# Kernel optimization log

Hardware: AMD Instinct MI355X
Metric: run time of the kernel (lower is better)

Reference implementation:

```python
import jax, jax.numpy as jnp
import numpy as np

INPUT_DIM = 2048
NUM_EXPERTS = 64
TOP_K = 8
BATCH = 16384


def setup_inputs() -> dict:
    key = jax.random.key(0)
    k_x, k_n, k_wg, k_bg, k_wn = jax.random.split(key, 5)
    x = jax.random.normal(k_x, (BATCH, INPUT_DIM), dtype=jnp.float32)
    noise = jax.random.normal(k_n, (BATCH, NUM_EXPERTS), dtype=jnp.float32)
    Wg = jax.random.normal(k_wg, (NUM_EXPERTS, INPUT_DIM), dtype=jnp.float32) * 0.02
    bg = jax.random.normal(k_bg, (NUM_EXPERTS,), dtype=jnp.float32) * 0.02
    Wn = jax.random.normal(k_wn, (NUM_EXPERTS, INPUT_DIM), dtype=jnp.float32) * 0.02
    return {"x": x, "noise": noise, "Wg": Wg, "bg": bg, "Wn": Wn}


def reference(x, noise, Wg, bg, Wn):
    # logits: (B, E)
    logits = jnp.einsum("bd,ed->be", x, Wg) + bg
    noise_stddev = jax.nn.softplus(jnp.einsum("bd,ed->be", x, Wn))
    noisy_logits = logits + noise * noise_stddev

    top_k_values, top_k_indices = jax.lax.top_k(noisy_logits, TOP_K)  # (B, K)
    top_k_weights = jax.nn.softmax(top_k_values, axis=-1)

    # aux losses
    dispatch = jnp.argmax(noisy_logits, axis=-1)            # (B,)
    f = jax.nn.one_hot(dispatch, NUM_EXPERTS, dtype=logits.dtype).mean(axis=0)  # (E,)
    p = jax.nn.softmax(logits, axis=-1).mean(axis=0)        # (E,)
    load_balance_loss = NUM_EXPERTS * jnp.sum(f * p)
    z_loss = jnp.mean(jax.nn.logsumexp(logits, axis=-1) ** 2)

    return top_k_weights, top_k_indices, load_balance_loss, z_loss
```

## Files before the change

kernel.cpp:

```cpp
#include <hip/hip_runtime.h>
#include <math.h>

#define IDIM 2048
#define NE   64
#define TOPK 8
#define NB   16384
#define BM   32
#define BK   64
#define NCH  (IDIM / BK)
#define KH   1024
#define NCHH 16
#define TAU  2.5e-4f

#define WS_CNT 129
#define WS_LIST 130
#define WSPLIT_BYTE 66560
#define WSPLIT_REQ  (WSPLIT_BYTE + NCH * 32768)
#define PART0_BYTE  (WSPLIT_BYTE + NCH * 32768)
#define PART1_BYTE  (PART0_BYTE + (size_t)NB * 128 * 4)
#define SPLIT_REQ   (PART1_BYTE + (size_t)NB * 128 * 4)

typedef __attribute__((ext_vector_type(8))) short bf16x8_t;
typedef __attribute__((ext_vector_type(4))) float f32x4_t;

__device__ __forceinline__ float softplusf(float v) {
    return (v > 0.f) ? (v + log1pf(expf(-v))) : log1pf(expf(v));
}
__device__ __forceinline__ double softplus_d(double v) {
    return (v > 0.0) ? (v + log1p(exp(-v))) : log1p(exp(v));
}

__device__ __forceinline__ short f2bf(float f) {
    unsigned u = __float_as_uint(f);
    unsigned r = (u + 0x7FFFu + ((u >> 16) & 1u)) >> 16;
    return (short)r;
}
__device__ __forceinline__ float bf2f(short s) {
    return __uint_as_float(((unsigned)(unsigned short)s) << 16);
}

__global__ void init_ws_kernel(float* ws) {
    int t = threadIdx.x;
    if (t < WS_LIST) ws[t] = 0.0f;
}

__device__ __forceinline__ void split8(const float4 v0, const float4 v1,
                                       bf16x8_t& H, bf16x8_t& L) {
    float fv[8] = {v0.x, v0.y, v0.z, v0.w, v1.x, v1.y, v1.z, v1.w};
    #pragma unroll
    for (int q = 0; q < 8; ++q) {
        short hb = f2bf(fv[q]);
        short lb = f2bf(fv[q] - bf2f(hb));
        H[q] = hb; L[q] = lb;
    }
}

__device__ __forceinline__ void cvt_slot(const float4 v0, const float4 v1,
                                         char* hiP, char* loP, int off) {
    bf16x8_t H, L;
    split8(v0, v1, H, L);
    *(bf16x8_t*)(hiP + off) = H;
    *(bf16x8_t*)(loP + off) = L;
}

__global__ __launch_bounds__(256) void prep_kernel(
    const float* __restrict__ Wg, const float* __restrict__ Wn,
    char* __restrict__ wsW, float* __restrict__ ws)
{
    if (blockIdx.x == 128) {
        if (threadIdx.x < WS_LIST) ws[threadIdx.x] = 0.0f;
        return;
    }
    int g = blockIdx.x * 256 + threadIdx.x;
    int t = g >> 10, i = g & 1023;
    int row = i >> 3, wslot = i & 7;
    int kslot = wslot ^ (row & 7);
    const float* src = (row < 64 ? Wg + (size_t)row * IDIM
                                 : Wn + (size_t)(row - 64) * IDIM) + t * BK + kslot * 8;
    float4 v0 = *(const float4*)src;
    float4 v1 = *(const float4*)(src + 4);
    bf16x8_t H, L;
    split8(v0, v1, H, L);
    char* dst = wsW + (size_t)t * 32768;
    *(bf16x8_t*)(dst + i * 16)         = H;
    *(bf16x8_t*)(dst + 16384 + i * 16) = L;
}

__global__ __launch_bounds__(512, 4) void gemm_half_kernel(
    const float* __restrict__ x, const char* __restrict__ wsW,
    float* __restrict__ part0, float* __restrict__ part1)
{
    __shared__ char smem[40960] __attribute__((aligned(16)));
    char* AH = smem;
    char* AL = smem + 4096;
    char* BH = smem + 8192;
    char* BL = smem + 24576;

    const int u   = threadIdx.x;
    const int w   = u >> 6;
    const int l   = u & 63;
    const int lr  = l & 15;
    const int lg4 = l >> 4;
    const int s7  = lr & 7;
    const int half = blockIdx.x & 1;
    const int row0 = (blockIdx.x >> 1) * BM;
    float* pb = half ? part1 : part0;

    const int ar  = (u >> 3) & 31;
    const int ac  = u & 7;
    const int aoff = ar * 128 + (((ac ^ (ar & 7)) & 7) << 4);
    const float* pa = x + (size_t)(row0 + ar) * IDIM + half * KH + ac * 8;

    f32x4_t acc[2];
    #pragma unroll
    for (int mt = 0; mt < 2; ++mt) {
        f32x4_t z = {0.f, 0.f, 0.f, 0.f};
        acc[mt] = z;
    }

    float4 ra0, ra1;
    int4 w0, w1, w2, w3;

#define HLOADT(tt) { const int k0 = (tt) * BK;                                  \
    if (u < 256) { ra0 = *(const float4*)(pa + k0);                             \
                   ra1 = *(const float4*)(pa + k0 + 4); }                       \
    const char* s_ = wsW + (size_t)(half * NCHH + (tt)) * 32768 + u * 16;       \
    w0 = *(const int4*)(s_);          w1 = *(const int4*)(s_ + 8192);           \
    w2 = *(const int4*)(s_ + 16384);  w3 = *(const int4*)(s_ + 24576); }

    HLOADT(0);

    for (int t = 0; t < NCHH; ++t) {
        __syncthreads();
        if (u < 256) cvt_slot(ra0, ra1, AH, AL, aoff);
        *(int4*)(BH + u * 16)        = w0;
        *(int4*)(BH + 8192 + u * 16) = w1;
        *(int4*)(BL + u * 16)        = w2;
        *(int4*)(BL + 8192 + u * 16) = w3;
        if (t + 1 < NCHH) HLOADT(t + 1);
        __syncthreads();

        #pragma unroll
        for (int ks = 0; ks < 2; ++ks) {
            const int so = (((ks * 4 + lg4) ^ s7) << 4);
            bf16x8_t ah[2], al_[2], bh, bl;
            #pragma unroll
            for (int mt = 0; mt < 2; ++mt) {
                const int o = (mt * 16 + lr) * 128 + so;
                ah[mt]  = *(const bf16x8_t*)(AH + o);
                al_[mt] = *(const bf16x8_t*)(AL + o);
            }
            {
                const int o = (w * 16 + lr) * 128 + so;
                bh = *(const bf16x8_t*)(BH + o);
                bl = *(const bf16x8_t*)(BL + o);
            }
            #pragma unroll
            for (int mt = 0; mt < 2; ++mt) {
                acc[mt] = __builtin_amdgcn_mfma_f32_16x16x32_bf16(ah[mt],  bh, acc[mt], 0, 0, 0);
                acc[mt] = __builtin_amdgcn_mfma_f32_16x16x32_bf16(ah[mt],  bl, acc[mt], 0, 0, 0);
                acc[mt] = __builtin_amdgcn_mfma_f32_16x16x32_bf16(al_[mt], bh, acc[mt], 0, 0, 0);
            }
        }
    }

    #pragma unroll
    for (int mt = 0; mt < 2; ++mt)
        #pragma unroll
        for (int r = 0; r < 4; ++r)
            pb[(size_t)(row0 + mt * 16 + lg4 * 4 + r) * 128 + (w * 16 + lr)] = acc[mt][r];
}

__global__ __launch_bounds__(512) void gating_kernel(
    const float* __restrict__ part0, const float* __restrict__ part1,
    const float* __restrict__ noise, const float* __restrict__ bg,
    float* __restrict__ out_w, float* __restrict__ out_i,
    float* __restrict__ ws, int listCap)
{
    __shared__ float sP[NE];
    __shared__ float sF[NE];
    __shared__ float sZ[1];
    const int u = threadIdx.x;
    const int w = u >> 6, l = u & 63;
    const int row0 = blockIdx.x * 32;

    if (u < NE) { sP[u] = 0.f; sF[u] = 0.f; }
    if (u == 0) sZ[0] = 0.f;
    __syncthreads();

    float pacc = 0.f, zacc = 0.f;
    #pragma unroll 1
    for (int rr = 0; rr < 4; ++rr) {
        const int grow = row0 + w * 4 + rr;
        float lg   = part0[(size_t)grow * 128 + l] + part1[(size_t)grow * 128 + l] + bg[l];
        float npre = part0[(size_t)grow * 128 + 64 + l] + part1[(size_t)grow * 128 + 64 + l];
        float vcur = fmaf(noise[(size_t)grow * NE + l], softplusf(npre), lg);

        float tkv[9]; int tki[9];
        #pragma unroll
        for (int k = 0; k < 9; ++k) {
            float mv = vcur; int mi = l;
            #pragma unroll
            for (int o = 32; o > 0; o >>= 1) {
                float ov = __shfl_xor(mv, o);
                int   oi = __shfl_xor(mi, o);
                if (ov > mv || (ov == mv && oi < mi)) { mv = ov; mi = oi; }
            }
            tkv[k] = mv; tki[k] = mi;
            if (l == mi) vcur = -1e30f;
        }

        float m0 = tkv[0], s = 0.f, wk[TOPK];
        #pragma unroll
        for (int k = 0; k < TOPK; ++k) { wk[k] = expf(tkv[k] - m0); s += wk[k]; }
        float inv = 1.f / s;
        float myw = 0.f; int myi = 0;
        #pragma unroll
        for (int k = 0; k < TOPK; ++k)
            if (l == k) { myw = wk[k] * inv; myi = tki[k]; }
        if (l < TOPK) {
            out_w[(size_t)grow * TOPK + l] = myw;
            out_i[(size_t)grow * TOPK + l] = (float)myi;
        }

        if (l == 0) {
            atomicAdd(&sF[tki[0]], 1.f);
            float ming = 1e30f;
            #pragma unroll
            for (int k = 0; k < 8; ++k) ming = fminf(ming, tkv[k] - tkv[k + 1]);
            if (ming < TAU) {
                int slot = atomicAdd((int*)&ws[WS_CNT], 1);
                if (slot < listCap) ((int*)ws)[WS_LIST + slot] = grow;
            }
        }

        float rm = lg;
        #pragma unroll
        for (int o = 32; o > 0; o >>= 1) rm = fmaxf(rm, __shfl_xor(rm, o));
        float pe = expf(lg - rm);
        float ssum = pe;
        #pragma unroll
        for (int o = 32; o > 0; o >>= 1) ssum += __shfl_xor(ssum, o);
        pacc += pe / ssum;
        if (l == 0) { float lse = rm + logf(ssum); zacc += lse * lse; }
    }

    atomicAdd(&sP[l], pacc);
    if (l == 0) atomicAdd(sZ, zacc);
    __syncthreads();
    if (u < NE) {
        atomicAdd(&ws[u],      sF[u]);
        atomicAdd(&ws[NE + u], sP[u]);
    }
    if (u == 0) atomicAdd(&ws[2 * NE], sZ[0]);
}

template<bool PRE>
__global__ __launch_bounds__(512, 4) void gate_main_kernel(
    const float* __restrict__ x, const float* __restrict__ noise,
    const float* __restrict__ Wg, const float* __restrict__ bg,
    const float* __restrict__ Wn, const char* __restrict__ wsW,
    float* __restrict__ out_w, float* __restrict__ out_i,
    float* __restrict__ ws, int listCap)
{
    __shared__ char smem[41488] __attribute__((aligned(16)));
    char* AH = smem;
    char* AL = smem + 4096;
    char* BH = smem + 8192;
    char* BL = smem + 24576;
    float* sP = (float*)(smem + 40960);
    float* sF = (float*)(smem + 41216);
    float* sZ = (float*)(smem + 41472);
    float* sL = (float*)smem;

    const int u   = threadIdx.x;
    const int w   = u >> 6;
    const int l   = u & 63;
    const int lr  = l & 15;
    const int lg4 = l >> 4;
    const int s7  = lr & 7;
    const int row0 = blockIdx.x * BM;

    if (u < NE) { sP[u] = 0.f; sF[u] = 0.f; }
    if (u == 0) sZ[0] = 0.f;

    const int ar  = (u >> 3) & 31;
    const int ac  = u & 7;
    const int aoff = ar * 128 + (((ac ^ (ar & 7)) & 7) << 4);
    const float* pa = x + (size_t)(row0 + ar) * IDIM + ac * 8;

    const int br  = u >> 3;
    const float* pg = Wg + (size_t)br * IDIM + ac * 8;
    const float* pn = Wn + (size_t)br * IDIM + ac * 8;
    const int woff = br * 128 + ((ac ^ (br & 7)) << 4);

    f32x4_t acc[2];
    #pragma unroll
    for (int mt = 0; mt < 2; ++mt) {
        f32x4_t z = {0.f, 0.f, 0.f, 0.f};
        acc[mt] = z;
    }

    float4 ra0, ra1;
    int4 w0, w1, w2, w3;
    float4 g0, g1, n0, n1;

#define LOADT(tt) { const int k0 = (tt) * BK;                                   \
    if (u < 256) { ra0 = *(const float4*)(pa + k0);                             \
                   ra1 = *(const float4*)(pa + k0 + 4); }                       \
    if constexpr (PRE) {                                                        \
        const char* s_ = wsW + (size_t)(tt) * 32768 + u * 16;                   \
        w0 = *(const int4*)(s_);          w1 = *(const int4*)(s_ + 8192);       \
        w2 = *(const int4*)(s_ + 16384);  w3 = *(const int4*)(s_ + 24576);      \
    } else {                                                                    \
        g0 = *(const float4*)(pg + k0);   g1 = *(const float4*)(pg + k0 + 4);   \
        n0 = *(const float4*)(pn + k0);   n1 = *(const float4*)(pn + k0 + 4);   \
    } }

    LOADT(0);

    for (int t = 0; t < NCH; ++t) {
        __syncthreads();
        if (u < 256) cvt_slot(ra0, ra1, AH, AL, aoff);
        if constexpr (PRE) {
            *(int4*)(BH + u * 16)        = w0;
            *(int4*)(BH + 8192 + u * 16) = w1;
            *(int4*)(BL + u * 16)        = w2;
            *(int4*)(BL + 8192 + u * 16) = w3;
        } else {
            cvt_slot(g0, g1, BH, BL, woff);
            cvt_slot(n0, n1, BH, BL, woff + 8192);
        }
        if (t + 1 < NCH) LOADT(t + 1);
        __syncthreads();

        #pragma unroll
        for (int ks = 0; ks < 2; ++ks) {
            const int so = (((ks * 4 + lg4) ^ s7) << 4);
            bf16x8_t ah[2], al_[2], bh, bl;
            #pragma unroll
            for (int mt = 0; mt < 2; ++mt) {
                const int o = (mt * 16 + lr) * 128 + so;
                ah[mt]  = *(const bf16x8_t*)(AH + o);
                al_[mt] = *(const bf16x8_t*)(AL + o);
            }
            {
                const int o = (w * 16 + lr) * 128 + so;
                bh = *(const bf16x8_t*)(BH + o);
                bl = *(const bf16x8_t*)(BL + o);
            }
            #pragma unroll
            for (int mt = 0; mt < 2; ++mt) {
                acc[mt] = __builtin_amdgcn_mfma_f32_16x16x32_bf16(ah[mt],  bh, acc[mt], 0, 0, 0);
                acc[mt] = __builtin_amdgcn_mfma_f32_16x16x32_bf16(ah[mt],  bl, acc[mt], 0, 0, 0);
                acc[mt] = __builtin_amdgcn_mfma_f32_16x16x32_bf16(al_[mt], bh, acc[mt], 0, 0, 0);
            }
        }
    }
    __syncthreads();

    #pragma unroll
    for (int mt = 0; mt < 2; ++mt)
        #pragma unroll
        for (int r = 0; r < 4; ++r)
            sL[(mt * 16 + lg4 * 4 + r) * 132 + (w * 16 + lr)] = acc[mt][r];
    __syncthreads();

    float pacc = 0.f, zacc = 0.f;
    #pragma unroll 1
    for (int rr = 0; rr < 4; ++rr) {
        const int r = w * 4 + rr;
        const int grow = row0 + r;
        float lg   = sL[r * 132 + l] + bg[l];
        float npre = sL[r * 132 + 64 + l];
        float vcur = fmaf(noise[(size_t)grow * NE + l], softplusf(npre), lg);

        float tkv[9]; int tki[9];
        #pragma unroll
        for (int k = 0; k < 9; ++k) {
            float mv = vcur; int mi = l;
            #pragma unroll
            for (int o = 32; o > 0; o >>= 1) {
                float ov = __shfl_xor(mv, o);
                int   oi = __shfl_xor(mi, o);
                if (ov > mv || (ov == mv && oi < mi)) { mv = ov; mi = oi; }
            }
            tkv[k] = mv; tki[k] = mi;
            if (l == mi) vcur = -1e30f;
        }

        float m0 = tkv[0], s = 0.f, wk[TOPK];
        #pragma unroll
        for (int k = 0; k < TOPK; ++k) { wk[k] = expf(tkv[k] - m0); s += wk[k]; }
        float inv = 1.f / s;
        float myw = 0.f; int myi = 0;
        #pragma unroll
        for (int k = 0; k < TOPK; ++k)
            if (l == k) { myw = wk[k] * inv; myi = tki[k]; }
        if (l < TOPK) {
            out_w[(size_t)grow * TOPK + l] = myw;
            out_i[(size_t)grow * TOPK + l] = (float)myi;
        }

        if (l == 0) {
            atomicAdd(&sF[tki[0]], 1.f);
            float ming = 1e30f;
            #pragma unroll
            for (int k = 0; k < 8; ++k) ming = fminf(ming, tkv[k] - tkv[k + 1]);
            if (ming < TAU) {
                int slot = atomicAdd((int*)&ws[WS_CNT], 1);
                if (slot < listCap) ((int*)ws)[WS_LIST + slot] = grow;
            }
        }

        float rm = lg;
        #pragma unroll
        for (int o = 32; o > 0; o >>= 1) rm = fmaxf(rm, __shfl_xor(rm, o));
        float pe = expf(lg - rm);
        float ssum = pe;
        #pragma unroll
        for (int o = 32; o > 0; o >>= 1) ssum += __shfl_xor(ssum, o);
        pacc += pe / ssum;
        if (l == 0) { float lse = rm + logf(ssum); zacc += lse * lse; }
    }

    atomicAdd(&sP[l], pacc);
    if (l == 0) atomicAdd(sZ, zacc);
    __syncthreads();
    if (u < NE) {
        atomicAdd(&ws[u],      sF[u]);
        atomicAdd(&ws[NE + u], sP[u]);
    }
    if (u == 0) atomicAdd(&ws[2 * NE], sZ[0]);
}

__global__ __launch_bounds__(512) void recheck_finalize_kernel(
    const float* __restrict__ x, const float* __restrict__ noise,
    const float* __restrict__ Wg, const float* __restrict__ bg,
    const float* __restrict__ Wn,
    float* __restrict__ out_w, float* __restrict__ out_i, float* __restrict__ out_s,
    const float* __restrict__ ws, int listCap)
{
    __shared__ double sRed[1024];
    const int t = threadIdx.x;

    if (blockIdx.x == 0 && t < 64) {
        float v = (ws[t] / (float)NB) * (ws[NE + t] / (float)NB);
        #pragma unroll
        for (int o = 32; o > 0; o >>= 1) v += __shfl_down(v, o);
        if (t == 0) {
            out_s[0] = (float)NE * v;
            out_s[1] = ws[2 * NE] / (float)NB;
        }
    }

    const int* wsi = (const int*)ws;
    int cnt = wsi[WS_CNT];
    if (cnt > listCap) cnt = listCap;
    if (cnt <= 0) return;

    const int slot = t & 127;
    const int q4   = t >> 7;
    const float* wrb = ((slot < 64) ? (Wg + (size_t)slot * IDIM)
                                    : (Wn + (size_t)(slot - 64) * IDIM)) + q4 * 512;

    const int npair = (cnt + 1) >> 1;
    for (int bi = blockIdx.x; bi < npair; bi += gridDim.x) {
        const int i1 = 2 * bi + 1;
        const int r0 = wsi[WS_LIST + 2 * bi];
        const int r1 = wsi[WS_LIST + (i1 < cnt ? i1 : cnt - 1)];
        const float* x0 = x + (size_t)r0 * IDIM + q4 * 512;
        const float* x1 = x + (size_t)r1 * IDIM + q4 * 512;

        double a0 = 0.0, a1 = 0.0;
        #pragma unroll 4
        for (int k = 0; k < 512; k += 4) {
            float4 wv  = *(const float4*)(wrb + k);
            float4 xv0 = *(const float4*)(x0 + k);
            float4 xv1 = *(const float4*)(x1 + k);
            a0 = fma((double)xv0.x, (double)wv.x, a0);
            a1 = fma((double)xv1.x, (double)wv.x, a1);
            a0 = fma((double)xv0.y, (double)wv.y, a0);
            a1 = fma((double)xv1.y, (double)wv.y, a1);
            a0 = fma((double)xv0.z, (double)wv.z, a0);
            a1 = fma((double)xv1.z, (double)wv.z, a1);
            a0 = fma((double)xv0.w, (double)wv.w, a0);
            a1 = fma((double)xv1.w, (double)wv.w, a1);
        }
        sRed[t * 2]     = a0;
        sRed[t * 2 + 1] = a1;
        __syncthreads();
        if (t < 128) {
            #pragma unroll
            for (int i = 0; i < 2; ++i)
                sRed[t * 2 + i] = sRed[t * 2 + i] + sRed[(t + 128) * 2 + i]
                                + sRed[(t + 256) * 2 + i] + sRed[(t + 384) * 2 + i];
        }
        __syncthreads();

        if (t < 64) {
            const int lane = t;
            const double bgl = (double)bg[lane];
            #pragma unroll 1
            for (int i = 0; i < 2; ++i) {
                const int row = i ? r1 : r0;
                double g = sRed[lane * 2 + i];
                double n = sRed[(64 + lane) * 2 + i];
                double lgd = g + bgl;
                double nz = (double)noise[(size_t)row * NE + lane];
                double vcur = fma(nz, softplus_d(n), lgd);

                double tkv[TOPK]; int tki[TOPK];
                #pragma unroll
                for (int k = 0; k < TOPK; ++k) {
                    double mv = vcur; int mi = lane;
                    #pragma unroll
                    for (int o = 32; o > 0; o >>= 1) {
                        double ov = __shfl_xor(mv, o);
                        int    oi = __shfl_xor(mi, o);
                        if (ov > mv || (ov == mv && oi < mi)) { mv = ov; mi = oi; }
                    }
                    tkv[k] = mv; tki[k] = mi;
                    if (lane == mi) vcur = -1e300;
                }
                double m0 = tkv[0], s = 0.0, wk[TOPK];
                #pragma unroll
                for (int k = 0; k < TOPK; ++k) { wk[k] = exp(tkv[k] - m0); s += wk[k]; }
                double inv = 1.0 / s;
                float myw = 0.f; int myi = 0;
                #pragma unroll
                for (int k = 0; k < TOPK; ++k)
                    if (lane == k) { myw = (float)(wk[k] * inv); myi = tki[k]; }
                if (lane < TOPK) {
                    out_w[(size_t)row * TOPK + lane] = myw;
                    out_i[(size_t)row * TOPK + lane] = (float)myi;
                }
            }
        }
        __syncthreads();
    }
}

extern "C" void kernel_launch(void* const* d_in, const int* in_sizes, int n_in,
                              void* d_out, int out_size, void* d_ws, size_t ws_size,
                              hipStream_t stream) {
    const float* x     = (const float*)d_in[0];
    const float* noise = (const float*)d_in[1];
    const float* Wg    = (const float*)d_in[2];
    const float* bg    = (const float*)d_in[3];
    const float* Wn    = (const float*)d_in[4];
    float* out = (float*)d_out;
    float* ws  = (float*)d_ws;
    char*  wsW = (char*)d_ws + WSPLIT_BYTE;

    long cap = (long)(ws_size / 4) - WS_LIST;
    int listCap = (int)(cap < 0 ? 0 : (cap > NB ? NB : cap));
    const bool pre   = ws_size >= (size_t)WSPLIT_REQ;
    const bool split = ws_size >= (size_t)SPLIT_REQ;

    if (split) {
        float* part0 = (float*)((char*)d_ws + PART0_BYTE);
        float* part1 = (float*)((char*)d_ws + PART1_BYTE);
        hipLaunchKernelGGL(prep_kernel, dim3(129), dim3(256), 0, stream, Wg, Wn, wsW, ws);
        hipLaunchKernelGGL(gemm_half_kernel, dim3(2 * NB / BM), dim3(512), 0, stream,
                           x, wsW, part0, part1);
        hipLaunchKernelGGL(gating_kernel, dim3(NB / 32), dim3(512), 0, stream,
                           part0, part1, noise, bg,
                           out, out + (size_t)NB * TOPK, ws, listCap);
    } else if (pre) {
        hipLaunchKernelGGL(prep_kernel, dim3(129), dim3(256), 0, stream, Wg, Wn, wsW, ws);
        hipLaunchKernelGGL(gate_main_kernel<true>, dim3(NB / BM), dim3(512), 0, stream,
                           x, noise, Wg, bg, Wn, wsW,
                           out, out + (size_t)NB * TOPK, ws, listCap);
    } else {
        hipLaunchKernelGGL(init_ws_kernel, dim3(1), dim3(256), 0, stream, ws);
        hipLaunchKernelGGL(gate_main_kernel<false>, dim3(NB / BM), dim3(512), 0, stream,
                           x, noise, Wg, bg, Wn, wsW,
                           out, out + (size_t)NB * TOPK, ws, listCap);
    }
    hipLaunchKernelGGL(recheck_finalize_kernel, dim3(1024), dim3(512), 0, stream,
                       x, noise, Wg, bg, Wn,
                       out, out + (size_t)NB * TOPK, out + 2 * (size_t)NB * TOPK,
                       ws, listCap);
}
```

Baseline: 144.8 us.

## Split GEMM reduction dimension into four parts and widen recheck blocks

The split-K GEMM now splits the 2048-wide reduction into four 512-wide slices instead of two, launching four times as many blocks per row tile, each doing half as many K chunks. The gating kernel sums four partial buffers, which doubles partial-result traffic in exchange for more parallelism. The recheck/finalize kernel moves to 1024-thread blocks, each thread covering 256 K elements, and does an 8-way shared reduction. TAU drops to 1e-4, which changes how many rows are flagged for the fp64 recheck and could shrink the recheck list.

```diff
diff --git a/kernel.cpp b/kernel.cpp
--- a/kernel.cpp
+++ b/kernel.cpp
@@ -8,17 +8,17 @@
 #define BM   32
 #define BK   64
 #define NCH  (IDIM / BK)
-#define KH   1024
-#define NCHH 16
-#define TAU  2.5e-4f
+#define NQ   4
+#define KQ   512
+#define NCHQ 8
+#define TAU  1e-4f
 
 #define WS_CNT 129
 #define WS_LIST 130
 #define WSPLIT_BYTE 66560
 #define WSPLIT_REQ  (WSPLIT_BYTE + NCH * 32768)
-#define PART0_BYTE  (WSPLIT_BYTE + NCH * 32768)
-#define PART1_BYTE  (PART0_BYTE + (size_t)NB * 128 * 4)
-#define SPLIT_REQ   (PART1_BYTE + (size_t)NB * 128 * 4)
+#define PART_BYTE   (WSPLIT_BYTE + NCH * 32768)
+#define SPLIT_REQ   (PART_BYTE + (size_t)NQ * NB * 128 * 4)
 
 typedef __attribute__((ext_vector_type(8))) short bf16x8_t;
 typedef __attribute__((ext_vector_type(4))) float f32x4_t;
@@ -86,9 +86,9 @@
     *(bf16x8_t*)(dst + 16384 + i * 16) = L;
 }
 
-__global__ __launch_bounds__(512, 4) void gemm_half_kernel(
+__global__ __launch_bounds__(512, 4) void gemm_quarter_kernel(
     const float* __restrict__ x, const char* __restrict__ wsW,
-    float* __restrict__ part0, float* __restrict__ part1)
+    float* __restrict__ part)
 {
     __shared__ char smem[40960] __attribute__((aligned(16)));
     char* AH = smem;
@@ -102,14 +102,14 @@
     const int lr  = l & 15;
     const int lg4 = l >> 4;
     const int s7  = lr & 7;
-    const int half = blockIdx.x & 1;
-    const int row0 = (blockIdx.x >> 1) * BM;
-    float* pb = half ? part1 : part0;
+    const int q   = blockIdx.x & 3;
+    const int row0 = (blockIdx.x >> 2) * BM;
+    float* pb = part + (size_t)q * NB * 128;
 
     const int ar  = (u >> 3) & 31;
     const int ac  = u & 7;
     const int aoff = ar * 128 + (((ac ^ (ar & 7)) & 7) << 4);
-    const float* pa = x + (size_t)(row0 + ar) * IDIM + half * KH + ac * 8;
+    const float* pa = x + (size_t)(row0 + ar) * IDIM + q * KQ + ac * 8;
 
     f32x4_t acc[2];
     #pragma unroll
@@ -121,23 +121,23 @@
     float4 ra0, ra1;
     int4 w0, w1, w2, w3;
 
-#define HLOADT(tt) { const int k0 = (tt) * BK;                                  \
+#define QLOADT(tt) { const int k0 = (tt) * BK;                                  \
     if (u < 256) { ra0 = *(const float4*)(pa + k0);                             \
                    ra1 = *(const float4*)(pa + k0 + 4); }                       \
-    const char* s_ = wsW + (size_t)(half * NCHH + (tt)) * 32768 + u * 16;       \
+    const char* s_ = wsW + (size_t)(q * NCHQ + (tt)) * 32768 + u * 16;          \
     w0 = *(const int4*)(s_);          w1 = *(const int4*)(s_ + 8192);           \
     w2 = *(const int4*)(s_ + 16384);  w3 = *(const int4*)(s_ + 24576); }
 
-    HLOADT(0);
-
-    for (int t = 0; t < NCHH; ++t) {
+    QLOADT(0);
+
+    for (int t = 0; t < NCHQ; ++t) {
         __syncthreads();
         if (u < 256) cvt_slot(ra0, ra1, AH, AL, aoff);
         *(int4*)(BH + u * 16)        = w0;
         *(int4*)(BH + 8192 + u * 16) = w1;
         *(int4*)(BL + u * 16)        = w2;
         *(int4*)(BL + 8192 + u * 16) = w3;
-        if (t + 1 < NCHH) HLOADT(t + 1);
+        if (t + 1 < NCHQ) QLOADT(t + 1);
         __syncthreads();
 
         #pragma unroll
@@ -172,7 +172,7 @@
 }
 
 __global__ __launch_bounds__(512) void gating_kernel(
-    const float* __restrict__ part0, const float* __restrict__ part1,
+    const float* __restrict__ part,
     const float* __restrict__ noise, const float* __restrict__ bg,
     float* __restrict__ out_w, float* __restrict__ out_i,
     float* __restrict__ ws, int listCap)
@@ -183,6 +183,10 @@
     const int u = threadIdx.x;
     const int w = u >> 6, l = u & 63;
     const int row0 = blockIdx.x * 32;
+    const float* p0 = part;
+    const float* p1 = part + (size_t)NB * 128;
+    const float* p2 = part + 2 * (size_t)NB * 128;
+    const float* p3 = part + 3 * (size_t)NB * 128;
 
     if (u < NE) { sP[u] = 0.f; sF[u] = 0.f; }
     if (u == 0) sZ[0] = 0.f;
@@ -192,8 +196,9 @@
     #pragma unroll 1
     for (int rr = 0; rr < 4; ++rr) {
         const int grow = row0 + w * 4 + rr;
-        float lg   = part0[(size_t)grow * 128 + l] + part1[(size_t)grow * 128 + l] + bg[l];
-        float npre = part0[(size_t)grow * 128 + 64 + l] + part1[(size_t)grow * 128 + 64 + l];
+        const size_t b = (size_t)grow * 128;
+        float lg   = ((p0[b + l] + p1[b + l]) + (p2[b + l] + p3[b + l])) + bg[l];
+        float npre = (p0[b + 64 + l] + p1[b + 64 + l]) + (p2[b + 64 + l] + p3[b + 64 + l]);
         float vcur = fmaf(noise[(size_t)grow * NE + l], softplusf(npre), lg);
 
         float tkv[9]; int tki[9];
@@ -434,14 +439,14 @@
     if (u == 0) atomicAdd(&ws[2 * NE], sZ[0]);
 }
 
-__global__ __launch_bounds__(512) void recheck_finalize_kernel(
+__global__ __launch_bounds__(1024) void recheck_finalize_kernel(
     const float* __restrict__ x, const float* __restrict__ noise,
     const float* __restrict__ Wg, const float* __restrict__ bg,
     const float* __restrict__ Wn,
     float* __restrict__ out_w, float* __restrict__ out_i, float* __restrict__ out_s,
     const float* __restrict__ ws, int listCap)
 {
-    __shared__ double sRed[1024];
+    __shared__ double sRed[2048];
     const int t = threadIdx.x;
 
     if (blockIdx.x == 0 && t < 64) {
@@ -460,21 +465,21 @@
     if (cnt <= 0) return;
 
     const int slot = t & 127;
-    const int q4   = t >> 7;
+    const int kg   = t >> 7;
     const float* wrb = ((slot < 64) ? (Wg + (size_t)slot * IDIM)
-                                    : (Wn + (size_t)(slot - 64) * IDIM)) + q4 * 512;
+                                    : (Wn + (size_t)(slot - 64) * IDIM)) + kg * 256;
 
     const int npair = (cnt + 1) >> 1;
     for (int bi = blockIdx.x; bi < npair; bi += gridDim.x) {
         const int i1 = 2 * bi + 1;
         const int r0 = wsi[WS_LIST + 2 * bi];
         const int r1 = wsi[WS_LIST + (i1 < cnt ? i1 : cnt - 1)];
-        const float* x0 = x + (size_t)r0 * IDIM + q4 * 512;
-        const float* x1 = x + (size_t)r1 * IDIM + q4 * 512;
+        const float* x0 = x + (size_t)r0 * IDIM + kg * 256;
+        const float* x1 = x + (size_t)r1 * IDIM + kg * 256;
 
         double a0 = 0.0, a1 = 0.0;
         #pragma unroll 4
-        for (int k = 0; k < 512; k += 4) {
+        for (int k = 0; k < 256; k += 4) {
             float4 wv  = *(const float4*)(wrb + k);
             float4 xv0 = *(const float4*)(x0 + k);
             float4 xv1 = *(const float4*)(x1 + k);
@@ -491,10 +496,14 @@
         sRed[t * 2 + 1] = a1;
         __syncthreads();
         if (t < 128) {
-            #pragma unroll
-            for (int i = 0; i < 2; ++i)
-                sRed[t * 2 + i] = sRed[t * 2 + i] + sRed[(t + 128) * 2 + i]
-                                + sRed[(t + 256) * 2 + i] + sRed[(t + 384) * 2 + i];
+            double s0 = 0.0, s1 = 0.0;
+            #pragma unroll
+            for (int g = 0; g < 8; ++g) {
+                s0 += sRed[(g * 128 + t) * 2];
+                s1 += sRed[(g * 128 + t) * 2 + 1];
+            }
+            sRed[t * 2]     = s0;
+            sRed[t * 2 + 1] = s1;
         }
         __syncthreads();
 
@@ -559,13 +568,12 @@
     const bool split = ws_size >= (size_t)SPLIT_REQ;
 
     if (split) {
-        float* part0 = (float*)((char*)d_ws + PART0_BYTE);
-        float* part1 = (float*)((char*)d_ws + PART1_BYTE);
+        float* part = (float*)((char*)d_ws + PART_BYTE);
         hipLaunchKernelGGL(prep_kernel, dim3(129), dim3(256), 0, stream, Wg, Wn, wsW, ws);
-        hipLaunchKernelGGL(gemm_half_kernel, dim3(2 * NB / BM), dim3(512), 0, stream,
-                           x, wsW, part0, part1);
+        hipLaunchKernelGGL(gemm_quarter_kernel, dim3(NQ * NB / BM), dim3(512), 0, stream,
+                           x, wsW, part);
         hipLaunchKernelGGL(gating_kernel, dim3(NB / 32), dim3(512), 0, stream,
-                           part0, part1, noise, bg,
+                           part, noise, bg,
                            out, out + (size_t)NB * TOPK, ws, listCap);
     } else if (pre) {
         hipLaunchKernelGGL(prep_kernel, dim3(129), dim3(256), 0, stream, Wg, Wn, wsW, ws);
@@ -578,7 +586,7 @@
                            x, noise, Wg, bg, Wn, wsW,
                            out, out + (size_t)NB * TOPK, ws, listCap);
     }
-    hipLaunchKernelGGL(recheck_finalize_kernel, dim3(1024), dim3(512), 0, stream,
+    hipLaunchKernelGGL(recheck_finalize_kernel, dim3(1024), dim3(1024), 0, stream,
                        x, noise, Wg, bg, Wn,
                        out, out + (size_t)NB * TOPK, out + 2 * (size_t)NB * TOPK,
                        ws, listCap);
```

Measured after the change: 146.6 us. Within noise of the previous version (+1.3%).
